# Kernel tuning notes

Hardware: AMD Instinct MI355X
Metric: run time of the kernel (lower is better)

Reference implementation:

```python
import jax, jax.numpy as jnp
import numpy as np

B, STATE_DIM, HIDDEN, ACTION_DIM = 262144, 128, 256, 8


def setup_inputs() -> dict:
    key = jax.random.key(0)
    ks = jax.random.split(key, 5)
    state = jax.random.normal(ks[0], (B, STATE_DIM), dtype=jnp.float32)
    # torch init: weight.data.normal_(0, 0.01); biases left at default -> zeros here
    W1 = jax.random.normal(ks[1], (HIDDEN, STATE_DIM), dtype=jnp.float32) * 0.01
    b1 = jnp.zeros((HIDDEN,), dtype=jnp.float32)
    W2 = jax.random.normal(ks[2], (HIDDEN, HIDDEN), dtype=jnp.float32) * 0.01
    b2 = jnp.zeros((HIDDEN,), dtype=jnp.float32)
    W3 = jax.random.normal(ks[3], (2 * ACTION_DIM, HIDDEN), dtype=jnp.float32) * 0.01
    b3 = jnp.zeros((2 * ACTION_DIM,), dtype=jnp.float32)
    # reparameterized noise for torch.normal(u, s): sample = u + |s| * eps
    eps = jax.random.normal(ks[4], (B, ACTION_DIM), dtype=jnp.float32)
    return {"state": state, "W1": W1, "b1": b1, "W2": W2, "b2": b2,
            "W3": W3, "b3": b3, "eps": eps}


def reference(state, W1, b1, W2, b2, W3, b3, eps):
    x = state.reshape(-1, STATE_DIM)
    h = jax.nn.relu(x @ W1.T + b1)
    h = jax.nn.relu(h @ W2.T + b2)
    n = h @ W3.T + b3                       # [B, 2*ACTION_DIM]
    u = n[:, :ACTION_DIM]                   # mean
    s = jnp.abs(n[:, ACTION_DIM:])          # std (abs as in np.abs)
    action = jax.nn.sigmoid(u + s * eps)    # sigmoid(normal(u, s))
    return (action * 8 + 1).astype(jnp.int32)  # (action*8+1).int(), per row
```

## Files before the change

kernel.cpp:

```cpp
#include <hip/hip_runtime.h>
#include <math.h>

#define NB  262144
#define SD  128
#define HID 256
#define AD  8

typedef float v2f __attribute__((ext_vector_type(2)));

#define W1T_OFF 0
#define W2T_OFF (SD*HID)
#define W3P_OFF (W2T_OFF + HID*HID)
#define B1_OFF  (W3P_OFF + HID*2*AD)
#define B2_OFF  (B1_OFF + HID)
#define B3P_OFF (B2_OFF + HID)
#define WS_FLOATS (B3P_OFF + 2*AD)

__global__ __launch_bounds__(256) void prep_weights(
    const float* __restrict__ W1, const float* __restrict__ b1,
    const float* __restrict__ W2, const float* __restrict__ b2,
    const float* __restrict__ W3, const float* __restrict__ b3,
    float* __restrict__ ws) {
  int stride = gridDim.x * blockDim.x;
  for (int i = blockIdx.x * blockDim.x + threadIdx.x; i < WS_FLOATS; i += stride) {
    float v;
    if (i < W2T_OFF) {
      int k = i >> 8, j = i & 255;
      v = W1[j * SD + k];
    } else if (i < W3P_OFF) {
      int t = i - W2T_OFF;
      int k = t >> 8, j = t & 255;
      v = W2[j * HID + k];
    } else if (i < B1_OFF) {
      int t = i - W3P_OFF;
      int k = t >> 4, a = (t >> 1) & 7, h = t & 1;
      v = W3[(a + 8 * h) * HID + k];
    } else if (i < B2_OFF) {
      v = b1[i - B1_OFF];
    } else if (i < B3P_OFF) {
      v = b2[i - B2_OFF];
    } else {
      int t = i - B3P_OFF;
      v = b3[(t >> 1) + 8 * (t & 1)];
    }
    ws[i] = v;
  }
}


__global__ __launch_bounds__(256, 3) void actor_fused(
    const float* __restrict__ state, const float* __restrict__ eps,
    const float* __restrict__ ws, int* __restrict__ out) {
  __shared__ float s_h[32][264];

  const int tid  = threadIdx.x;
  const int lane = tid & 63;
  const int wvu  = __builtin_amdgcn_readfirstlane(tid >> 6);
  const long wrow = (long)blockIdx.x * 32 + wvu * 8;

  const float4* __restrict__ W1T4 = (const float4*)(ws + W1T_OFF);
  const float4* __restrict__ W2T4 = (const float4*)(ws + W2T_OFF);
  const v2f*    __restrict__ W3P  = (const v2f*)(ws + W3P_OFF);

  const float* __restrict__ xbase = state + wrow * SD;

  float acc[8][4];
  #pragma unroll
  for (int r = 0; r < 8; ++r)
    #pragma unroll
    for (int c = 0; c < 4; ++c) acc[r][c] = 0.0f;

  #pragma unroll 2
  for (int k0 = 0; k0 < SD; k0 += 4) {
    float4 w[4];
    #pragma unroll
    for (int j = 0; j < 4; ++j) w[j] = W1T4[(k0 + j) * 64 + lane];
    float4 xv[8];
    #pragma unroll
    for (int r = 0; r < 8; ++r)
      xv[r] = *(const float4*)(xbase + r * SD + k0);
    #pragma unroll
    for (int j = 0; j < 4; ++j) {
      #pragma unroll
      for (int r = 0; r < 8; ++r) {
        float x = (j == 0) ? xv[r].x : (j == 1) ? xv[r].y
                : (j == 2) ? xv[r].z : xv[r].w;
        acc[r][0] = fmaf(x, w[j].x, acc[r][0]);
        acc[r][1] = fmaf(x, w[j].y, acc[r][1]);
        acc[r][2] = fmaf(x, w[j].z, acc[r][2]);
        acc[r][3] = fmaf(x, w[j].w, acc[r][3]);
      }
    }
  }

  {
    float4 bb = ((const float4*)(ws + B1_OFF))[lane];
    #pragma unroll
    for (int r = 0; r < 8; ++r) {
      float4 hv;
      hv.x = acc[r][0] + bb.x; hv.y = acc[r][1] + bb.y;
      hv.z = acc[r][2] + bb.z; hv.w = acc[r][3] + bb.w;
      hv.x = hv.x > 0.0f ? hv.x : 0.0f;
      hv.y = hv.y > 0.0f ? hv.y : 0.0f;
      hv.z = hv.z > 0.0f ? hv.z : 0.0f;
      hv.w = hv.w > 0.0f ? hv.w : 0.0f;
      *(float4*)&s_h[wvu * 8 + r][4 * lane] = hv;
    }
  }

  #pragma unroll
  for (int r = 0; r < 8; ++r)
    #pragma unroll
    for (int c = 0; c < 4; ++c) acc[r][c] = 0.0f;

  #pragma unroll 2
  for (int k0 = 0; k0 < HID; k0 += 4) {
    float4 w[4];
    #pragma unroll
    for (int j = 0; j < 4; ++j) w[j] = W2T4[(k0 + j) * 64 + lane];
    float4 xv[8];
    #pragma unroll
    for (int r = 0; r < 8; ++r)
      xv[r] = *(const float4*)&s_h[wvu * 8 + r][k0];
    #pragma unroll
    for (int j = 0; j < 4; ++j) {
      #pragma unroll
      for (int r = 0; r < 8; ++r) {
        float x = (j == 0) ? xv[r].x : (j == 1) ? xv[r].y
                : (j == 2) ? xv[r].z : xv[r].w;
        acc[r][0] = fmaf(x, w[j].x, acc[r][0]);
        acc[r][1] = fmaf(x, w[j].y, acc[r][1]);
        acc[r][2] = fmaf(x, w[j].z, acc[r][2]);
        acc[r][3] = fmaf(x, w[j].w, acc[r][3]);
      }
    }
  }

  {
    float4 bb = ((const float4*)(ws + B2_OFF))[lane];
    #pragma unroll
    for (int r = 0; r < 8; ++r) {
      float4 hv;
      hv.x = acc[r][0] + bb.x; hv.y = acc[r][1] + bb.y;
      hv.z = acc[r][2] + bb.z; hv.w = acc[r][3] + bb.w;
      hv.x = hv.x > 0.0f ? hv.x : 0.0f;
      hv.y = hv.y > 0.0f ? hv.y : 0.0f;
      hv.z = hv.z > 0.0f ? hv.z : 0.0f;
      hv.w = hv.w > 0.0f ? hv.w : 0.0f;
      *(float4*)&s_h[wvu * 8 + r][4 * lane] = hv;
    }
  }

  {
    const int r3 = lane >> 3;
    const int a  = lane & 7;
    const float* __restrict__ h2row = &s_h[wvu * 8 + r3][0];
    float accu = 0.0f, accs = 0.0f;
    #pragma unroll 2
    for (int k0 = 0; k0 < HID; k0 += 4) {
      v2f ha = *(const v2f*)(h2row + k0);
      v2f hb = *(const v2f*)(h2row + k0 + 2);
      v2f wp0 = W3P[(k0 + 0) * 8 + a];
      v2f wp1 = W3P[(k0 + 1) * 8 + a];
      v2f wp2 = W3P[(k0 + 2) * 8 + a];
      v2f wp3 = W3P[(k0 + 3) * 8 + a];
      accu = fmaf(ha.x, wp0.x, accu); accs = fmaf(ha.x, wp0.y, accs);
      accu = fmaf(ha.y, wp1.x, accu); accs = fmaf(ha.y, wp1.y, accs);
      accu = fmaf(hb.x, wp2.x, accu); accs = fmaf(hb.x, wp2.y, accs);
      accu = fmaf(hb.y, wp3.x, accu); accs = fmaf(hb.y, wp3.y, accs);
    }
    v2f b3p = ((const v2f*)(ws + B3P_OFF))[a];
    float nu = accu + b3p.x;
    float ns = accs + b3p.y;

    long grow = wrow + r3;
    float sa = fabsf(ns);
    float ev = eps[grow * AD + a];
    float t  = __fmul_rn(sa, ev);
    float z  = __fadd_rn(nu, t);
    float e  = (float)exp(-(double)z);
    float d  = __fadd_rn(1.0f, e);
    float act = 1.0f / d;
    float q  = act * 8.0f;
    float wq = __fadd_rn(q, 1.0f);
    out[grow * AD + a] = (int)wq;
  }
}

extern "C" void kernel_launch(void* const* d_in, const int* in_sizes, int n_in,
                              void* d_out, int out_size, void* d_ws, size_t ws_size,
                              hipStream_t stream) {
  const float* state = (const float*)d_in[0];
  const float* W1    = (const float*)d_in[1];
  const float* b1    = (const float*)d_in[2];
  const float* W2    = (const float*)d_in[3];
  const float* b2    = (const float*)d_in[4];
  const float* W3    = (const float*)d_in[5];
  const float* b3    = (const float*)d_in[6];
  const float* eps   = (const float*)d_in[7];
  int*   out = (int*)d_out;
  float* ws  = (float*)d_ws;

  hipLaunchKernelGGL(prep_weights, dim3(128), dim3(256), 0, stream,
                     W1, b1, W2, b2, W3, b3, ws);
  hipLaunchKernelGGL(actor_fused, dim3(NB / 32), dim3(256), 0, stream,
                     state, eps, ws, out);
}
```

Baseline: 871.2 us.

## Use packed FP32 FMA inline asm, XOR-swizzle hidden tile, raise occupancy

The scalar FMA inner loops of all three layers are replaced with v_pk_fma_f32 inline assembly, using op_sel to broadcast one input element across two accumulator lanes, which halves the FMA instruction count. The shared hidden buffer loses its padding and uses an XOR swizzle on the column index to avoid LDS bank conflicts, with reads adjusted to match. The launch-bounds occupancy hint rises from 3 to 5 waves per SIMD, which may tighten register allocation and cause spills. Inline asm hides the operations from the compiler's scheduler and may add moves to build the packed operands.

```diff
diff --git a/kernel.cpp b/kernel.cpp
--- a/kernel.cpp
+++ b/kernel.cpp
@@ -7,6 +7,7 @@
 #define AD  8
 
 typedef float v2f __attribute__((ext_vector_type(2)));
+typedef float v4f __attribute__((ext_vector_type(4)));
 
 #define W1T_OFF 0
 #define W2T_OFF (SD*HID)
@@ -48,106 +49,107 @@
 }
 
 
-__global__ __launch_bounds__(256, 3) void actor_fused(
+#define PK_LO(acc, x2, w2) \
+  asm("v_pk_fma_f32 %0, %1, %2, %0 op_sel:[0,0,0] op_sel_hi:[0,1,1]" \
+      : "+v"(acc) : "v"(x2), "v"(w2))
+#define PK_HI(acc, x2, w2) \
+  asm("v_pk_fma_f32 %0, %1, %2, %0 op_sel:[1,0,0] op_sel_hi:[1,1,1]" \
+      : "+v"(acc) : "v"(x2), "v"(w2))
+
+__global__ __launch_bounds__(256, 5) void actor_fused(
     const float* __restrict__ state, const float* __restrict__ eps,
     const float* __restrict__ ws, int* __restrict__ out) {
-  __shared__ float s_h[32][264];
+  __shared__ float s_h[32][256];
 
   const int tid  = threadIdx.x;
   const int lane = tid & 63;
   const int wvu  = __builtin_amdgcn_readfirstlane(tid >> 6);
   const long wrow = (long)blockIdx.x * 32 + wvu * 8;
 
-  const float4* __restrict__ W1T4 = (const float4*)(ws + W1T_OFF);
-  const float4* __restrict__ W2T4 = (const float4*)(ws + W2T_OFF);
-  const v2f*    __restrict__ W3P  = (const v2f*)(ws + W3P_OFF);
+  const v4f* __restrict__ W1T4 = (const v4f*)(ws + W1T_OFF);
+  const v4f* __restrict__ W2T4 = (const v4f*)(ws + W2T_OFF);
+  const v2f* __restrict__ W3P  = (const v2f*)(ws + W3P_OFF);
 
   const float* __restrict__ xbase = state + wrow * SD;
 
-  float acc[8][4];
+  v2f acc0[8], acc1[8];
   #pragma unroll
-  for (int r = 0; r < 8; ++r)
-    #pragma unroll
-    for (int c = 0; c < 4; ++c) acc[r][c] = 0.0f;
+  for (int r = 0; r < 8; ++r) { acc0[r] = (v2f){0.f, 0.f}; acc1[r] = (v2f){0.f, 0.f}; }
 
   #pragma unroll 2
   for (int k0 = 0; k0 < SD; k0 += 4) {
-    float4 w[4];
-    #pragma unroll
-    for (int j = 0; j < 4; ++j) w[j] = W1T4[(k0 + j) * 64 + lane];
-    float4 xv[8];
+    v4f w0 = W1T4[(k0 + 0) * 64 + lane];
+    v4f w1 = W1T4[(k0 + 1) * 64 + lane];
+    v4f w2 = W1T4[(k0 + 2) * 64 + lane];
+    v4f w3 = W1T4[(k0 + 3) * 64 + lane];
+    v2f w0l = w0.xy, w0h = w0.zw, w1l = w1.xy, w1h = w1.zw;
+    v2f w2l = w2.xy, w2h = w2.zw, w3l = w3.xy, w3h = w3.zw;
+    v4f xv[8];
     #pragma unroll
     for (int r = 0; r < 8; ++r)
-      xv[r] = *(const float4*)(xbase + r * SD + k0);
-    #pragma unroll
-    for (int j = 0; j < 4; ++j) {
-      #pragma unroll
-      for (int r = 0; r < 8; ++r) {
-        float x = (j == 0) ? xv[r].x : (j == 1) ? xv[r].y
-                : (j == 2) ? xv[r].z : xv[r].w;
-        acc[r][0] = fmaf(x, w[j].x, acc[r][0]);
-        acc[r][1] = fmaf(x, w[j].y, acc[r][1]);
-        acc[r][2] = fmaf(x, w[j].z, acc[r][2]);
-        acc[r][3] = fmaf(x, w[j].w, acc[r][3]);
-      }
+      xv[r] = *(const v4f*)(xbase + r * SD + k0);
+    #pragma unroll
+    for (int r = 0; r < 8; ++r) {
+      v2f x01 = xv[r].xy, x23 = xv[r].zw;
+      PK_LO(acc0[r], x01, w0l); PK_LO(acc1[r], x01, w0h);
+      PK_HI(acc0[r], x01, w1l); PK_HI(acc1[r], x01, w1h);
+      PK_LO(acc0[r], x23, w2l); PK_LO(acc1[r], x23, w2h);
+      PK_HI(acc0[r], x23, w3l); PK_HI(acc1[r], x23, w3h);
     }
   }
 
   {
-    float4 bb = ((const float4*)(ws + B1_OFF))[lane];
-    #pragma unroll
-    for (int r = 0; r < 8; ++r) {
-      float4 hv;
-      hv.x = acc[r][0] + bb.x; hv.y = acc[r][1] + bb.y;
-      hv.z = acc[r][2] + bb.z; hv.w = acc[r][3] + bb.w;
+    v4f bb = ((const v4f*)(ws + B1_OFF))[lane];
+    #pragma unroll
+    for (int r = 0; r < 8; ++r) {
+      v4f hv;
+      hv.x = acc0[r].x + bb.x; hv.y = acc0[r].y + bb.y;
+      hv.z = acc1[r].x + bb.z; hv.w = acc1[r].y + bb.w;
       hv.x = hv.x > 0.0f ? hv.x : 0.0f;
       hv.y = hv.y > 0.0f ? hv.y : 0.0f;
       hv.z = hv.z > 0.0f ? hv.z : 0.0f;
       hv.w = hv.w > 0.0f ? hv.w : 0.0f;
-      *(float4*)&s_h[wvu * 8 + r][4 * lane] = hv;
+      *(v4f*)&s_h[wvu * 8 + r][(lane ^ r) << 2] = hv;
     }
   }
 
   #pragma unroll
-  for (int r = 0; r < 8; ++r)
-    #pragma unroll
-    for (int c = 0; c < 4; ++c) acc[r][c] = 0.0f;
+  for (int r = 0; r < 8; ++r) { acc0[r] = (v2f){0.f, 0.f}; acc1[r] = (v2f){0.f, 0.f}; }
 
   #pragma unroll 2
   for (int k0 = 0; k0 < HID; k0 += 4) {
-    float4 w[4];
-    #pragma unroll
-    for (int j = 0; j < 4; ++j) w[j] = W2T4[(k0 + j) * 64 + lane];
-    float4 xv[8];
+    v4f w0 = W2T4[(k0 + 0) * 64 + lane];
+    v4f w1 = W2T4[(k0 + 1) * 64 + lane];
+    v4f w2 = W2T4[(k0 + 2) * 64 + lane];
+    v4f w3 = W2T4[(k0 + 3) * 64 + lane];
+    v2f w0l = w0.xy, w0h = w0.zw, w1l = w1.xy, w1h = w1.zw;
+    v2f w2l = w2.xy, w2h = w2.zw, w3l = w3.xy, w3h = w3.zw;
+    v4f xv[8];
     #pragma unroll
     for (int r = 0; r < 8; ++r)
-      xv[r] = *(const float4*)&s_h[wvu * 8 + r][k0];
-    #pragma unroll
-    for (int j = 0; j < 4; ++j) {
-      #pragma unroll
-      for (int r = 0; r < 8; ++r) {
-        float x = (j == 0) ? xv[r].x : (j == 1) ? xv[r].y
-                : (j == 2) ? xv[r].z : xv[r].w;
-        acc[r][0] = fmaf(x, w[j].x, acc[r][0]);
-        acc[r][1] = fmaf(x, w[j].y, acc[r][1]);
-        acc[r][2] = fmaf(x, w[j].z, acc[r][2]);
-        acc[r][3] = fmaf(x, w[j].w, acc[r][3]);
-      }
+      xv[r] = *(const v4f*)&s_h[wvu * 8 + r][(((k0 >> 2) ^ r) << 2)];
+    #pragma unroll
+    for (int r = 0; r < 8; ++r) {
+      v2f x01 = xv[r].xy, x23 = xv[r].zw;
+      PK_LO(acc0[r], x01, w0l); PK_LO(acc1[r], x01, w0h);
+      PK_HI(acc0[r], x01, w1l); PK_HI(acc1[r], x01, w1h);
+      PK_LO(acc0[r], x23, w2l); PK_LO(acc1[r], x23, w2h);
+      PK_HI(acc0[r], x23, w3l); PK_HI(acc1[r], x23, w3h);
     }
   }
 
   {
-    float4 bb = ((const float4*)(ws + B2_OFF))[lane];
-    #pragma unroll
-    for (int r = 0; r < 8; ++r) {
-      float4 hv;
-      hv.x = acc[r][0] + bb.x; hv.y = acc[r][1] + bb.y;
-      hv.z = acc[r][2] + bb.z; hv.w = acc[r][3] + bb.w;
+    v4f bb = ((const v4f*)(ws + B2_OFF))[lane];
+    #pragma unroll
+    for (int r = 0; r < 8; ++r) {
+      v4f hv;
+      hv.x = acc0[r].x + bb.x; hv.y = acc0[r].y + bb.y;
+      hv.z = acc1[r].x + bb.z; hv.w = acc1[r].y + bb.w;
       hv.x = hv.x > 0.0f ? hv.x : 0.0f;
       hv.y = hv.y > 0.0f ? hv.y : 0.0f;
       hv.z = hv.z > 0.0f ? hv.z : 0.0f;
       hv.w = hv.w > 0.0f ? hv.w : 0.0f;
-      *(float4*)&s_h[wvu * 8 + r][4 * lane] = hv;
+      *(v4f*)&s_h[wvu * 8 + r][(lane ^ r) << 2] = hv;
     }
   }
 
@@ -155,23 +157,24 @@
     const int r3 = lane >> 3;
     const int a  = lane & 7;
     const float* __restrict__ h2row = &s_h[wvu * 8 + r3][0];
-    float accu = 0.0f, accs = 0.0f;
+    v2f accus = (v2f){0.f, 0.f};
     #pragma unroll 2
     for (int k0 = 0; k0 < HID; k0 += 4) {
-      v2f ha = *(const v2f*)(h2row + k0);
-      v2f hb = *(const v2f*)(h2row + k0 + 2);
+      const int col = ((k0 >> 2) ^ r3) << 2;
+      v2f ha = *(const v2f*)(h2row + col);
+      v2f hb = *(const v2f*)(h2row + col + 2);
       v2f wp0 = W3P[(k0 + 0) * 8 + a];
       v2f wp1 = W3P[(k0 + 1) * 8 + a];
       v2f wp2 = W3P[(k0 + 2) * 8 + a];
       v2f wp3 = W3P[(k0 + 3) * 8 + a];
-      accu = fmaf(ha.x, wp0.x, accu); accs = fmaf(ha.x, wp0.y, accs);
-      accu = fmaf(ha.y, wp1.x, accu); accs = fmaf(ha.y, wp1.y, accs);
-      accu = fmaf(hb.x, wp2.x, accu); accs = fmaf(hb.x, wp2.y, accs);
-      accu = fmaf(hb.y, wp3.x, accu); accs = fmaf(hb.y, wp3.y, accs);
+      PK_LO(accus, ha, wp0);
+      PK_HI(accus, ha, wp1);
+      PK_LO(accus, hb, wp2);
+      PK_HI(accus, hb, wp3);
     }
     v2f b3p = ((const v2f*)(ws + B3P_OFF))[a];
-    float nu = accu + b3p.x;
-    float ns = accs + b3p.y;
+    float nu = accus.x + b3p.x;
+    float ns = accus.y + b3p.y;
 
     long grow = wrow + r3;
     float sa = fabsf(ns);
```

After: 892.5 us. 1.02x slower.
